# Kernel tuning notes

Hardware: AMD Instinct MI355X
Metric: run time of the kernel (lower is better)

The kernel has to match this reference:

```python
import jax, jax.numpy as jnp
import numpy as np

B, DIM, IN_DIM, H, W = 4, 512, 256, 64, 64
DOWN = IN_DIM // 2          # 128
QK = DOWN // 8              # 16
EPS = 1e-5


def conv2d(x, w, b, pad=0, dil=1):
    y = jax.lax.conv_general_dilated(
        x, w, window_strides=(1, 1),
        padding=[(pad, pad), (pad, pad)],
        rhs_dilation=(dil, dil),
        dimension_numbers=('NCHW', 'OIHW', 'NCHW'))
    return y + b[None, :, None, None]


def bn(x, g, bt, m, v):
    # inference-mode BatchNorm2d with running stats
    scale = (g * jax.lax.rsqrt(v + EPS))[None, :, None, None]
    return (x - m[None, :, None, None]) * scale + bt[None, :, None, None]


def prelu(x, a):
    return jnp.where(x >= 0, x, a * x)


def setup_inputs() -> dict:
    key = jax.random.key(0)
    ks = iter(jax.random.split(key, 64))
    d = {}
    d['x'] = jax.random.normal(next(ks), (B, DIM, H, W), dtype=jnp.float32)

    def conv_params(name, cout, cin, k):
        d[name + '_w'] = jax.random.normal(next(ks), (cout, cin, k, k), jnp.float32) * 0.05
        d[name + '_b'] = jax.random.normal(next(ks), (cout,), jnp.float32) * 0.05

    def bn_params(name, c):
        d[name + '_g'] = 1.0 + 0.1 * jax.random.normal(next(ks), (c,), jnp.float32)
        d[name + '_bt'] = 0.1 * jax.random.normal(next(ks), (c,), jnp.float32)
        d[name + '_m'] = 0.1 * jax.random.normal(next(ks), (c,), jnp.float32)
        d[name + '_v'] = 0.5 + jax.random.uniform(next(ks), (c,), jnp.float32)

    def prelu_param(name):
        d[name] = jnp.full((1,), 0.25, jnp.float32)

    conv_params('dc', IN_DIM, DIM, 3);  bn_params('dc_bn', IN_DIM); prelu_param('dc_a')
    conv_params('c1', DOWN, IN_DIM, 1); bn_params('c1_bn', DOWN);   prelu_param('c1_a')
    conv_params('c2', DOWN, IN_DIM, 3); bn_params('c2_bn', DOWN);   prelu_param('c2_a')
    conv_params('q', QK, DOWN, 1)
    conv_params('k', QK, DOWN, 1)
    conv_params('v', DOWN, DOWN, 1)
    d['gamma2'] = jnp.full((1,), 0.1, jnp.float32)  # torch init is 0; nonzero to exercise the path
    conv_params('c3', DOWN, IN_DIM, 1); bn_params('c3_bn', DOWN);   prelu_param('c3_a')
    conv_params('f', IN_DIM, 3 * DOWN, 1); bn_params('f_bn', IN_DIM); prelu_param('f_a')
    return d


def reference(x,
              dc_w, dc_b, dc_bn_g, dc_bn_bt, dc_bn_m, dc_bn_v, dc_a,
              c1_w, c1_b, c1_bn_g, c1_bn_bt, c1_bn_m, c1_bn_v, c1_a,
              c2_w, c2_b, c2_bn_g, c2_bn_bt, c2_bn_m, c2_bn_v, c2_a,
              q_w, q_b, k_w, k_b, v_w, v_b, gamma2,
              c3_w, c3_b, c3_bn_g, c3_bn_bt, c3_bn_m, c3_bn_v, c3_a,
              f_w, f_b, f_bn_g, f_bn_bt, f_bn_m, f_bn_v, f_a):
    # down_conv: 3x3 conv + BN + PReLU
    x = prelu(bn(conv2d(x, dc_w, dc_b, pad=1), dc_bn_g, dc_bn_bt, dc_bn_m, dc_bn_v), dc_a)
    # branch 1: 1x1 conv
    c1 = prelu(bn(conv2d(x, c1_w, c1_b), c1_bn_g, c1_bn_bt, c1_bn_m, c1_bn_v), c1_a)
    # branch 2: dilated 3x3 conv + non-local self-attention
    c2 = prelu(bn(conv2d(x, c2_w, c2_b, pad=2, dil=2), c2_bn_g, c2_bn_bt, c2_bn_m, c2_bn_v), c2_a)
    b, c, h, w = c2.shape
    hw = h * w
    q = conv2d(c2, q_w, q_b).reshape(b, QK, hw)   # [B, C/8, HW]
    k = conv2d(c2, k_w, k_b).reshape(b, QK, hw)
    v = conv2d(c2, v_w, v_b).reshape(b, c, hw)
    energy = jnp.einsum('bcn,bcm->bnm', q, k)     # [B, HW, HW]
    attn = jax.nn.softmax(energy, axis=-1)
    out2 = jnp.einsum('bcm,bnm->bcn', v, attn).reshape(b, c, h, w)
    out2 = gamma2 * out2 + c2
    # branch 3: global avg pool -> 1x1 conv -> broadcast (bilinear upsample of 1x1 is constant)
    pooled = jnp.mean(x, axis=(2, 3), keepdims=True)  # [B, IN_DIM, 1, 1]
    c3 = prelu(bn(conv2d(pooled, c3_w, c3_b), c3_bn_g, c3_bn_bt, c3_bn_m, c3_bn_v), c3_a)
    c3 = jnp.broadcast_to(c3, (b, DOWN, h, w))
    # fuse
    cat = jnp.concatenate([c1, out2, c3], axis=1)
    return prelu(bn(conv2d(cat, f_w, f_b), f_bn_g, f_bn_bt, f_bn_m, f_bn_v), f_a)
```

## Files before the change

### kernel.cpp

```cpp
#include <hip/hip_runtime.h>
#include <hip/hip_bf16.h>
#include <math.h>

#define HW 4096
#define EPSV 1e-5f

typedef unsigned short ushort;
typedef __attribute__((ext_vector_type(8))) short bf16x8;
typedef __attribute__((ext_vector_type(4))) float f32x4;

__device__ inline ushort f2bf(float f) {
    __hip_bfloat16 h = __float2bfloat16(f);
    return *reinterpret_cast<ushort*>(&h);
}
__device__ inline float bf2f(ushort u) {
    unsigned int v = ((unsigned int)u) << 16;
    return __uint_as_float(v);
}

template<int C>
__global__ __launch_bounds__(256) void to_chlast_bf16(
    const float* __restrict__ src, ushort* __restrict__ dst)
{
    const int b = blockIdx.z, c0 = blockIdx.y * 64, p0 = blockIdx.x * 64;
    const int tid = threadIdx.x;
    __shared__ float sT[64][65];
    for (int i = tid; i < 4096; i += 256) {
        const int ch = i >> 6, px = i & 63;
        sT[ch][px] = src[(size_t)(b * C + c0 + ch) * HW + p0 + px];
    }
    __syncthreads();
    const int px = tid >> 2, seg = tid & 3;
    ushort tmp[16];
    #pragma unroll
    for (int j = 0; j < 16; ++j) tmp[j] = f2bf(sT[seg * 16 + j][px]);
    ushort* d = dst + (size_t)(b * HW + p0 + px) * C + c0 + seg * 16;
    *(uint4*)d = *(uint4*)&tmp[0];
    *(uint4*)(d + 8) = *(uint4*)&tmp[8];
}

__global__ __launch_bounds__(256) void pack_all(
    const float* __restrict__ dc_w, ushort* __restrict__ wdcp,
    const float* __restrict__ c2_w, ushort* __restrict__ wc2p,
    const float* __restrict__ c1_w, ushort* __restrict__ wc1b,
    const float* __restrict__ f_w,  ushort* __restrict__ wfb,
    float* __restrict__ pool)
{
    constexpr int T_DC = 9 * 16 * 256 * 32;
    constexpr int T_C2 = 9 * 8 * 128 * 32;
    constexpr int T_C1 = 32768;
    constexpr int T_F  = 65536;
    int idx = blockIdx.x * 256 + threadIdx.x;
    if (idx < T_DC) {
        const int ci_in = idx & 31;
        int rest = idx >> 5;
        const int co = rest % 256; rest /= 256;
        const int cc = rest % 16;
        const int tap = rest / 16;
        wdcp[idx] = f2bf(dc_w[((size_t)co * 512 + cc * 32 + ci_in) * 9 + tap]);
        return;
    }
    idx -= T_DC;
    if (idx < T_C2) {
        const int ci_in = idx & 31;
        int rest = idx >> 5;
        const int co = rest % 128; rest /= 128;
        const int cc = rest % 8;
        const int tap = rest / 8;
        wc2p[idx] = f2bf(c2_w[((size_t)co * 256 + cc * 32 + ci_in) * 9 + tap]);
        return;
    }
    idx -= T_C2;
    if (idx < T_C1) {
        wc1b[idx] = f2bf(c1_w[idx]);
        return;
    }
    idx -= T_C1;
    if (idx < T_F) {
        const int co = idx >> 8, k = idx & 255;
        wfb[idx] = f2bf(f_w[co * 384 + k]);
        return;
    }
    idx -= T_F;
    if (idx < 1024) pool[idx] = 0.f;
}

template<int CIN, int COUT, int COTILE, int DIL, int ROWS, int OMODE>
__global__ __launch_bounds__(256, OMODE == 0 ? 4 : 2) void conv3x3_fused(
    const ushort* __restrict__ xin,
    const ushort* __restrict__ wpk,
    const float* __restrict__ bias, const float* __restrict__ bng,
    const float* __restrict__ bnb, const float* __restrict__ bnm,
    const float* __restrict__ bnv, const float* __restrict__ al,
    void* __restrict__ outv,
    float* __restrict__ pool)
{
    constexpr int HR = ROWS + 2 * DIL;
    constexpr int NC = 64 + 2 * DIL;
    constexpr int MT = COTILE / 16;
    constexpr int WPR = 4 / ROWS;
    constexpr int NT = ROWS;
    constexpr int SAS = 40;
    constexpr int CH = CIN / 32;
    constexpr int NA = HR * NC * 4;
    constexpr int NREG = (NA + 255) / 256;
    constexpr int WCH = 9 * MT * 64;
    constexpr int WPT = (WCH + 255) / 256;

    const int tid = threadIdx.x;
    const int wave = tid >> 6, lane = tid & 63;
    const int l15 = lane & 15, quad = lane >> 4;
    const int b = blockIdx.z;
    const int cob = blockIdx.y;
    const int co0 = cob * COTILE;
    const int h0 = blockIdx.x * ROWS;
    const int row = wave / WPR;
    const int ntbase = (wave % WPR) * NT;

    __shared__ __align__(16) ushort sA[HR * NC * SAS];
    __shared__ __align__(16) ushort sW[WCH * 8];

    f32x4 acc[MT][NT];
    #pragma unroll
    for (int mt = 0; mt < MT; ++mt)
        #pragma unroll
        for (int nt = 0; nt < NT; ++nt) acc[mt][nt] = (f32x4){0.f, 0.f, 0.f, 0.f};

    #pragma unroll 1
    for (int cc = 0; cc < CH; ++cc) {
        if (cc != 0) __syncthreads();
        #pragma unroll
        for (int k = 0; k < NREG; ++k) {
            const int i = tid + k * 256;
            if (i < NA) {
                const int p = i >> 2, seg = i & 3;
                const int r = p / NC, c = p - r * NC;
                const int grow = h0 - DIL + r, gcol = c - DIL;
                uint4 val = {0u, 0u, 0u, 0u};
                if (grow >= 0 && grow < 64 && gcol >= 0 && gcol < 64)
                    val = *(const uint4*)&xin[((size_t)(b * 64 + grow) * 64 + gcol) * CIN
                                              + cc * 32 + seg * 8];
                *(uint4*)&sA[p * SAS + seg * 8] = val;
            }
        }
        #pragma unroll
        for (int k = 0; k < WPT; ++k) {
            const int i = tid + k * 256;
            if (i < WCH) {
                const int tap = i / (MT * 64);
                const int r = i - tap * (MT * 64);
                const int mt = r >> 6, n = r & 63;
                const uint4 wv = *(const uint4*)&wpk[
                    ((size_t)(tap * (CIN / 32) + cc) * COUT + co0 + mt * 16 + (n & 15)) * 32
                    + (n >> 4) * 8];
                *(uint4*)&sW[i * 8] = wv;
            }
        }
        __syncthreads();

        #pragma unroll
        for (int tap = 0; tap < 9; ++tap) {
            const int ty = tap / 3, tx = tap - ty * 3;
            const int rl = row + ty * DIL;
            bf16x8 wf[MT];
            #pragma unroll
            for (int mt = 0; mt < MT; ++mt)
                wf[mt] = *(const bf16x8*)&sW[((tap * MT + mt) * 64 + lane) * 8];
            #pragma unroll
            for (int nt = 0; nt < NT; ++nt) {
                const int cl = (ntbase + nt) * 16 + l15 + tx * DIL;
                const bf16x8 bp = *(const bf16x8*)&sA[(rl * NC + cl) * SAS + quad * 8];
                #pragma unroll
                for (int mt = 0; mt < MT; ++mt)
                    acc[mt][nt] = __builtin_amdgcn_mfma_f32_16x16x32_bf16(
                        wf[mt], bp, acc[mt][nt], 0, 0, 0);
            }
        }
    }

    const float a = al[0];

    if constexpr (OMODE == 0) {
        __syncthreads();
        ushort* sT = sA;
        #pragma unroll
        for (int mt = 0; mt < MT; ++mt) {
            float sc[4], sh[4], psum[4];
            #pragma unroll
            for (int rr = 0; rr < 4; ++rr) {
                const int co = co0 + mt * 16 + quad * 4 + rr;
                sc[rr] = bng[co] * rsqrtf(bnv[co] + EPSV);
                sh[rr] = (bias[co] - bnm[co]) * sc[rr] + bnb[co];
                psum[rr] = 0.f;
            }
            #pragma unroll
            for (int nt = 0; nt < NT; ++nt) {
                float tv[4];
                #pragma unroll
                for (int rr = 0; rr < 4; ++rr) {
                    float t = acc[mt][nt][rr] * sc[rr] + sh[rr];
                    t = t >= 0.f ? t : a * t;
                    tv[rr] = t;
                    psum[rr] += t;
                }
                ushort4 u;
                u.x = f2bf(tv[0]); u.y = f2bf(tv[1]);
                u.z = f2bf(tv[2]); u.w = f2bf(tv[3]);
                const int px = (ntbase + nt) * 16 + l15;
                *(ushort4*)&sT[(row * 64 + px) * 40 + mt * 16 + quad * 4] = u;
            }
            #pragma unroll
            for (int rr = 0; rr < 4; ++rr) {
                float v = psum[rr];
                v += __shfl_xor(v, 1);
                v += __shfl_xor(v, 2);
                v += __shfl_xor(v, 4);
                v += __shfl_xor(v, 8);
                if (l15 == 0)
                    atomicAdd(&pool[b * 256 + co0 + mt * 16 + quad * 4 + rr], v);
            }
        }
        __syncthreads();
        ushort* dst = (ushort*)outv;
        const int p = tid >> 1, half = tid & 1;
        const uint4 v0 = *(const uint4*)&sT[p * 40 + half * 16];
        const uint4 v1 = *(const uint4*)&sT[p * 40 + half * 16 + 8];
        const size_t off = ((size_t)(b * 4096 + (h0 + (p >> 6)) * 64 + (p & 63))) * 256
                           + co0 + half * 16;
        *(uint4*)&dst[off] = v0;
        *(uint4*)&dst[off + 8] = v1;
    } else {
        float* out = (float*)outv;
        #pragma unroll
        for (int mt = 0; mt < MT; ++mt)
            #pragma unroll
            for (int rr = 0; rr < 4; ++rr) {
                const int co = co0 + mt * 16 + quad * 4 + rr;
                const float sc = bng[co] * rsqrtf(bnv[co] + EPSV);
                const float sh = (bias[co] - bnm[co]) * sc + bnb[co];
                #pragma unroll
                for (int nt = 0; nt < NT; ++nt) {
                    float t = acc[mt][nt][rr] * sc + sh;
                    t = t >= 0.f ? t : a * t;
                    out[((size_t)(b * COUT + co) * 64 + h0 + row) * 64
                        + (ntbase + nt) * 16 + l15] = t;
                }
            }
    }
}

template<int CIN, int COUT, bool BNACT, int OMODE>
__global__ __launch_bounds__(256) void gemm1x1_cl(
    const ushort* __restrict__ xin,
    const ushort* __restrict__ wbf,
    const float* __restrict__ bias, const float* __restrict__ bng,
    const float* __restrict__ bnb, const float* __restrict__ bnm,
    const float* __restrict__ bnv, const float* __restrict__ al,
    const float* __restrict__ ebias, void* __restrict__ outv,
    int ostride, int ocol)
{
    const int tid = threadIdx.x;
    const int wave = tid >> 6, lane = tid & 63;
    const int l15 = lane & 15, quad = lane >> 4;
    const int pix0 = blockIdx.x * 128 + wave * 32;
    const int co0 = blockIdx.y * 64;

    f32x4 acc[4][2];
    #pragma unroll
    for (int mt = 0; mt < 4; ++mt)
        #pragma unroll
        for (int nt = 0; nt < 2; ++nt) acc[mt][nt] = (f32x4){0.f, 0.f, 0.f, 0.f};

    #pragma unroll 2
    for (int cc = 0; cc < CIN / 32; ++cc) {
        bf16x8 aw[4], bp[2];
        #pragma unroll
        for (int mt = 0; mt < 4; ++mt)
            aw[mt] = *(const bf16x8*)&wbf[(size_t)(co0 + mt * 16 + l15) * CIN + cc * 32 + quad * 8];
        #pragma unroll
        for (int nt = 0; nt < 2; ++nt)
            bp[nt] = *(const bf16x8*)&xin[(size_t)(pix0 + nt * 16 + l15) * CIN + cc * 32 + quad * 8];
        #pragma unroll
        for (int mt = 0; mt < 4; ++mt)
            #pragma unroll
            for (int nt = 0; nt < 2; ++nt)
                acc[mt][nt] = __builtin_amdgcn_mfma_f32_16x16x32_bf16(
                    aw[mt], bp[nt], acc[mt][nt], 0, 0, 0);
    }

    const int bI = pix0 >> 12;
    const float a = BNACT ? al[0] : 0.f;

    if (OMODE == 0) {
        float* out = (float*)outv;
        #pragma unroll
        for (int mt = 0; mt < 4; ++mt)
            #pragma unroll
            for (int r = 0; r < 4; ++r) {
                const int co = co0 + mt * 16 + quad * 4 + r;
                float bb = bias[co];
                if (ebias) bb += ebias[bI * COUT + co];
                float scale = 1.f, shift = bb;
                if (BNACT) {
                    scale = bng[co] * rsqrtf(bnv[co] + EPSV);
                    shift = bb * scale + (bnb[co] - bnm[co] * scale);
                }
                #pragma unroll
                for (int nt = 0; nt < 2; ++nt) {
                    float t = acc[mt][nt][r] * scale + shift;
                    if (BNACT) t = t >= 0.f ? t : a * t;
                    out[((size_t)(bI * COUT + co)) * HW + (pix0 & 4095) + nt * 16 + l15] = t;
                }
            }
    } else {
        __shared__ ushort sT[4][32][68];
        #pragma unroll
        for (int mt = 0; mt < 4; ++mt)
            #pragma unroll
            for (int r = 0; r < 4; ++r) {
                const int co = co0 + mt * 16 + quad * 4 + r;
                float bb = bias[co];
                float scale = 1.f, shift = bb;
                if (BNACT) {
                    scale = bng[co] * rsqrtf(bnv[co] + EPSV);
                    shift = bb * scale + (bnb[co] - bnm[co] * scale);
                }
                #pragma unroll
                for (int nt = 0; nt < 2; ++nt) {
                    float t = acc[mt][nt][r] * scale + shift;
                    if (BNACT) t = t >= 0.f ? t : a * t;
                    sT[wave][nt * 16 + l15][mt * 16 + quad * 4 + r] = f2bf(t);
                }
            }
        __syncthreads();
        const int p = lane >> 1, half = lane & 1;
        ushort* out = (ushort*)outv;
        #pragma unroll
        for (int seg = 0; seg < 4; ++seg) {
            uint2 a0 = *(uint2*)&sT[wave][p][half * 32 + seg * 8];
            uint2 a1 = *(uint2*)&sT[wave][p][half * 32 + seg * 8 + 4];
            uint4 vv = {a0.x, a0.y, a1.x, a1.y};
            *(uint4*)&out[(size_t)(pix0 + p) * ostride + ocol + co0 + half * 32 + seg * 8] = vv;
        }
    }
}

__global__ __launch_bounds__(256) void c1_and_c3(
    const ushort* __restrict__ xin, const ushort* __restrict__ wbf,
    const float* __restrict__ bias, const float* __restrict__ bng,
    const float* __restrict__ bnb, const float* __restrict__ bnm,
    const float* __restrict__ bnv, const float* __restrict__ al,
    ushort* __restrict__ catb,
    const float* __restrict__ pool, const float* __restrict__ c3w,
    const float* __restrict__ c3b, const float* __restrict__ c3g,
    const float* __restrict__ c3bt, const float* __restrict__ c3m,
    const float* __restrict__ c3v, const float* __restrict__ c3a,
    const float* __restrict__ fw, float* __restrict__ fbias)
{
    const int tid = threadIdx.x;
    if (blockIdx.x >= 128) {
        const int b = (blockIdx.x - 128) * 2 + blockIdx.y;
        __shared__ float sp[256];
        __shared__ float sc3[128];
        sp[tid] = pool[b * 256 + tid] * (1.0f / 4096.0f);
        __syncthreads();
        if (tid < 128) {
            float acc2 = c3b[tid];
            for (int ci = 0; ci < 256; ++ci) acc2 = fmaf(c3w[tid * 256 + ci], sp[ci], acc2);
            const float scale = c3g[tid] * rsqrtf(c3v[tid] + EPSV);
            float t = (acc2 - c3m[tid]) * scale + c3bt[tid];
            const float a2 = c3a[0];
            sc3[tid] = t >= 0.f ? t : a2 * t;
        }
        __syncthreads();
        float f = 0.f;
        for (int j2 = 0; j2 < 128; ++j2) f = fmaf(fw[tid * 384 + 256 + j2], sc3[j2], f);
        fbias[b * 256 + tid] = f;
        return;
    }
    constexpr int CIN = 256;
    const int wave = tid >> 6, lane = tid & 63;
    const int l15 = lane & 15, quad = lane >> 4;
    const int pix0 = blockIdx.x * 128 + wave * 32;
    const int co0 = blockIdx.y * 64;

    f32x4 acc[4][2];
    #pragma unroll
    for (int mt = 0; mt < 4; ++mt)
        #pragma unroll
        for (int nt = 0; nt < 2; ++nt) acc[mt][nt] = (f32x4){0.f, 0.f, 0.f, 0.f};

    #pragma unroll 2
    for (int cc = 0; cc < CIN / 32; ++cc) {
        bf16x8 aw[4], bp[2];
        #pragma unroll
        for (int mt = 0; mt < 4; ++mt)
            aw[mt] = *(const bf16x8*)&wbf[(size_t)(co0 + mt * 16 + l15) * CIN + cc * 32 + quad * 8];
        #pragma unroll
        for (int nt = 0; nt < 2; ++nt)
            bp[nt] = *(const bf16x8*)&xin[(size_t)(pix0 + nt * 16 + l15) * CIN + cc * 32 + quad * 8];
        #pragma unroll
        for (int mt = 0; mt < 4; ++mt)
            #pragma unroll
            for (int nt = 0; nt < 2; ++nt)
                acc[mt][nt] = __builtin_amdgcn_mfma_f32_16x16x32_bf16(
                    aw[mt], bp[nt], acc[mt][nt], 0, 0, 0);
    }

    const float a = al[0];
    __shared__ ushort sT[4][32][68];
    #pragma unroll
    for (int mt = 0; mt < 4; ++mt)
        #pragma unroll
        for (int r = 0; r < 4; ++r) {
            const int co = co0 + mt * 16 + quad * 4 + r;
            const float scale = bng[co] * rsqrtf(bnv[co] + EPSV);
            const float shift = bias[co] * scale + (bnb[co] - bnm[co] * scale);
            #pragma unroll
            for (int nt = 0; nt < 2; ++nt) {
                float t = acc[mt][nt][r] * scale + shift;
                t = t >= 0.f ? t : a * t;
                sT[wave][nt * 16 + l15][mt * 16 + quad * 4 + r] = f2bf(t);
            }
        }
    __syncthreads();
    const int p = lane >> 1, half = lane & 1;
    #pragma unroll
    for (int seg = 0; seg < 4; ++seg) {
        uint2 a0 = *(uint2*)&sT[wave][p][half * 32 + seg * 8];
        uint2 a1 = *(uint2*)&sT[wave][p][half * 32 + seg * 8 + 4];
        uint4 vv = {a0.x, a0.y, a1.x, a1.y};
        *(uint4*)&catb[(size_t)(pix0 + p) * 256 + co0 + half * 32 + seg * 8] = vv;
    }
}

__global__ __launch_bounds__(256) void qkv_kernel(
    const float* __restrict__ c2g, const float* __restrict__ qw,
    const float* __restrict__ qb2, const float* __restrict__ kw,
    const float* __restrict__ kb2, ushort* __restrict__ qpack,
    ushort* __restrict__ kpack,
    const float* __restrict__ vw, const float* __restrict__ vb,
    ushort* __restrict__ vbh)
{
    const int tid = threadIdx.x;
    const int b = blockIdx.z, p0 = blockIdx.x * 64;
    __shared__ __align__(16) char smem[49152];

    if (blockIdx.y == 0) {
        float (*sC)[64]   = (float(*)[64])smem;
        float (*sWq)[128] = (float(*)[128])(smem + 32768);
        float (*sWk)[128] = (float(*)[128])(smem + 40960);
        for (int i = tid; i < 8192; i += 256) {
            const int px = i & 63, ci = i >> 6;
            sC[ci][px] = c2g[(size_t)(b * 128 + ci) * HW + p0 + px];
        }
        for (int i = tid; i < 2048; i += 256) {
            const int ci = i & 127, co = i >> 7;
            sWq[co][ci] = qw[co * 128 + ci];
            sWk[co][ci] = kw[co * 128 + ci];
        }
        __syncthreads();
        const int px = tid & 63, grp = tid >> 6;
        const int co0 = (grp & 1) * 8;
        const bool isK = grp >= 2;
        const float* sWp = isK ? &sWk[0][0] : &sWq[0][0];
        float acc[8] = {};
        for (int ci = 0; ci < 128; ++ci) {
            const float xv = sC[ci][px];
            #pragma unroll
            for (int j = 0; j < 8; ++j)
                acc[j] = fmaf(sWp[(co0 + j) * 128 + ci], xv, acc[j]);
        }
        const float* bsrc = isK ? kb2 : qb2;
        ushort* osrc = isK ? kpack : qpack;
        const size_t base = (size_t)(b * 4096 + p0 + px) * 32;
        #pragma unroll
        for (int j = 0; j < 8; ++j) {
            osrc[base + co0 + j] = f2bf(acc[j] + bsrc[co0 + j]);
            osrc[base + 16 + co0 + j] = 0;
        }
    } else {
        const int co0 = (blockIdx.y - 1) * 64;
        float* sIn = (float*)smem;
        float* sW  = (float*)(smem + 16384);
        const int cg = tid >> 4, pg = tid & 15;
        const int c0l = cg * 4, w0 = pg * 4;
        float acc[4][4] = {};
        for (int cc = 0; cc < 128; cc += 16) {
            {
                int i = tid;
                #pragma unroll
                for (int it = 0; it < 4; ++it, i += 256) {
                    const int px = i & 63, ci = i >> 6;
                    sIn[ci * 64 + px] = c2g[(size_t)(b * 128 + cc + ci) * HW + p0 + px];
                }
                i = tid;
                #pragma unroll
                for (int it = 0; it < 4; ++it, i += 256) {
                    const int ci = i & 15, co = i >> 4;
                    sW[ci * 68 + co] = vw[(co0 + co) * 128 + cc + ci];
                }
            }
            __syncthreads();
            #pragma unroll
            for (int ci = 0; ci < 16; ++ci) {
                const float4 iv = *(const float4*)&sIn[ci * 64 + w0];
                const float4 wv = *(const float4*)&sW[ci * 68 + c0l];
                const float ia[4] = {iv.x, iv.y, iv.z, iv.w};
                const float wa[4] = {wv.x, wv.y, wv.z, wv.w};
                #pragma unroll
                for (int i2 = 0; i2 < 4; ++i2)
                    #pragma unroll
                    for (int j = 0; j < 4; ++j)
                        acc[i2][j] = fmaf(wa[i2], ia[j], acc[i2][j]);
            }
            __syncthreads();
        }
        #pragma unroll
        for (int i2 = 0; i2 < 4; ++i2) {
            const int co = co0 + c0l + i2;
            const float shift = vb[co];
            const size_t base = (size_t)(b * 128 + co) * HW + p0 + w0;
            #pragma unroll
            for (int j = 0; j < 4; ++j)
                vbh[base + j] = f2bf(acc[i2][j] + shift);
        }
    }
}

__global__ __launch_bounds__(256) void attn_flash(
    const ushort* __restrict__ qpack,
    const ushort* __restrict__ kpack,
    const ushort* __restrict__ vpackT,
    ushort* __restrict__ opart,
    float* __restrict__ Mpart,
    float* __restrict__ Spart)
{
    const int tid = threadIdx.x;
    const int wave = tid >> 6, lane = tid & 63;
    const int l15 = lane & 15, quad = lane >> 4;
    const int b = blockIdx.z, j = blockIdx.y;
    const int n0w = blockIdx.x * 128 + wave * 32;
    const int m_begin = j * 512;

    __shared__ __align__(16) ushort sV[2][128][40];
    __shared__ __align__(16) ushort sP[4][2][16][40];

    const bf16x8 bq0 = *(const bf16x8*)(qpack + ((size_t)(b * 4096 + n0w + l15) * 32 + quad * 8));
    const bf16x8 bq1 = *(const bf16x8*)(qpack + ((size_t)(b * 4096 + n0w + 16 + l15) * 32 + quad * 8));
    const f32x4 z = {0.f, 0.f, 0.f, 0.f};

    float runM0 = -3e30f, runM1 = -3e30f;
    float runS0 = 0.f, runS1 = 0.f;
    f32x4 oacc0[8], oacc1[8];
    #pragma unroll
    for (int cs = 0; cs < 8; ++cs) {
        oacc0[cs] = (f32x4){0.f, 0.f, 0.f, 0.f};
        oacc1[cs] = (f32x4){0.f, 0.f, 0.f, 0.f};
    }

    const int stc = tid >> 1, stseg = tid & 1;

    {
        uint4 v0 = *(const uint4*)&vpackT[(size_t)(b * 128 + stc) * HW + m_begin + stseg * 16];
        uint4 v1 = *(const uint4*)&vpackT[(size_t)(b * 128 + stc) * HW + m_begin + stseg * 16 + 8];
        *(uint4*)&sV[0][stc][stseg * 16] = v0;
        *(uint4*)&sV[0][stc][stseg * 16 + 8] = v1;
    }
    __syncthreads();

    #pragma unroll 1
    for (int t = 0; t < 16; ++t) {
        const int m0 = m_begin + t * 32;
        const int buf = t & 1;
        uint4 nv0, nv1;
        const bool more = (t + 1 < 16);
        if (more) {
            const size_t nb = (size_t)(b * 128 + stc) * HW + m0 + 32 + stseg * 16;
            nv0 = *(const uint4*)&vpackT[nb];
            nv1 = *(const uint4*)&vpackT[nb + 8];
        }
        f32x4 s0[2], s1[2];
        #pragma unroll
        for (int ms = 0; ms < 2; ++ms) {
            const bf16x8 ak = *(const bf16x8*)(
                kpack + ((size_t)(b * 4096 + m0 + ms * 16 + l15) * 32 + quad * 8));
            s0[ms] = __builtin_amdgcn_mfma_f32_16x16x32_bf16(ak, bq0, z, 0, 0, 0);
            s1[ms] = __builtin_amdgcn_mfma_f32_16x16x32_bf16(ak, bq1, z, 0, 0, 0);
        }

        float tM0 = fmaxf(fmaxf(fmaxf(s0[0][0], s0[0][1]), fmaxf(s0[0][2], s0[0][3])),
                          fmaxf(fmaxf(s0[1][0], s0[1][1]), fmaxf(s0[1][2], s0[1][3])));
        float tM1 = fmaxf(fmaxf(fmaxf(s1[0][0], s1[0][1]), fmaxf(s1[0][2], s1[0][3])),
                          fmaxf(fmaxf(s1[1][0], s1[1][1]), fmaxf(s1[1][2], s1[1][3])));
        tM0 = fmaxf(tM0, __shfl_xor(tM0, 16));
        tM0 = fmaxf(tM0, __shfl_xor(tM0, 32));
        tM1 = fmaxf(tM1, __shfl_xor(tM1, 16));
        tM1 = fmaxf(tM1, __shfl_xor(tM1, 32));
        if (__any(tM0 > runM0 + 8.f)) {
            const float nM = fmaxf(runM0, tM0);
            const float sc = __builtin_amdgcn_exp2f((runM0 - nM) * 1.44269504f);
            runS0 *= sc;
            float scr[4];
            #pragma unroll
            for (int r = 0; r < 4; ++r) scr[r] = __shfl(sc, quad * 4 + r);
            #pragma unroll
            for (int cs = 0; cs < 8; ++cs) {
                oacc0[cs][0] *= scr[0]; oacc0[cs][1] *= scr[1];
                oacc0[cs][2] *= scr[2]; oacc0[cs][3] *= scr[3];
            }
            runM0 = nM;
        }
        if (__any(tM1 > runM1 + 8.f)) {
            const float nM = fmaxf(runM1, tM1);
            const float sc = __builtin_amdgcn_exp2f((runM1 - nM) * 1.44269504f);
            runS1 *= sc;
            float scr[4];
            #pragma unroll
            for (int r = 0; r < 4; ++r) scr[r] = __shfl(sc, quad * 4 + r);
            #pragma unroll
            for (int cs = 0; cs < 8; ++cs) {
                oacc1[cs][0] *= scr[0]; oacc1[cs][1] *= scr[1];
                oacc1[cs][2] *= scr[2]; oacc1[cs][3] *= scr[3];
            }
            runM1 = nM;
        }
        const float Ms0 = runM0 * 1.44269504f;
        const float Ms1 = runM1 * 1.44269504f;

        #pragma unroll
        for (int ms = 0; ms < 2; ++ms) {
            float p0[4], p1[4];
            #pragma unroll
            for (int r = 0; r < 4; ++r) {
                p0[r] = __builtin_amdgcn_exp2f(fmaf(s0[ms][r], 1.44269504f, -Ms0));
                p1[r] = __builtin_amdgcn_exp2f(fmaf(s1[ms][r], 1.44269504f, -Ms1));
                runS0 += p0[r];
                runS1 += p1[r];
            }
            ushort4 u0, u1;
            u0.x = f2bf(p0[0]); u0.y = f2bf(p0[1]); u0.z = f2bf(p0[2]); u0.w = f2bf(p0[3]);
            u1.x = f2bf(p1[0]); u1.y = f2bf(p1[1]); u1.z = f2bf(p1[2]); u1.w = f2bf(p1[3]);
            *(uint2*)&sP[wave][0][l15][ms * 16 + quad * 4] = *(uint2*)&u0;
            *(uint2*)&sP[wave][1][l15][ms * 16 + quad * 4] = *(uint2*)&u1;
        }
        asm volatile("s_waitcnt lgkmcnt(0)" ::: "memory");
        const bf16x8 ap0 = *(const bf16x8*)&sP[wave][0][l15][quad * 8];
        const bf16x8 ap1 = *(const bf16x8*)&sP[wave][1][l15][quad * 8];
        #pragma unroll
        for (int cs = 0; cs < 8; ++cs) {
            const bf16x8 bv = *(const bf16x8*)&sV[buf][cs * 16 + l15][quad * 8];
            oacc0[cs] = __builtin_amdgcn_mfma_f32_16x16x32_bf16(ap0, bv, oacc0[cs], 0, 0, 0);
            oacc1[cs] = __builtin_amdgcn_mfma_f32_16x16x32_bf16(ap1, bv, oacc1[cs], 0, 0, 0);
        }
        if (more) {
            *(uint4*)&sV[buf ^ 1][stc][stseg * 16] = nv0;
            *(uint4*)&sV[buf ^ 1][stc][stseg * 16 + 8] = nv1;
            __syncthreads();
        }
    }

    runS0 += __shfl_xor(runS0, 16);
    runS0 += __shfl_xor(runS0, 32);
    runS1 += __shfl_xor(runS1, 16);
    runS1 += __shfl_xor(runS1, 32);
    if (lane < 32) {
        const float Mv = (lane < 16) ? runM0 : runM1;
        const float Sv = (lane < 16) ? runS0 : runS1;
        const int n = n0w + ((lane < 16) ? 0 : 16) + l15;
        Mpart[((size_t)b * 8 + j) * 4096 + n] = Mv;
        Spart[((size_t)b * 8 + j) * 4096 + n] = Sv;
    }
    #pragma unroll
    for (int cs = 0; cs < 8; ++cs)
        #pragma unroll
        for (int r = 0; r < 4; ++r) {
            const int n = n0w + quad * 4 + r;
            opart[(((size_t)b * 8 + j) * 4096 + n) * 128 + cs * 16 + l15] = f2bf(oacc0[cs][r]);
            opart[(((size_t)b * 8 + j) * 4096 + n + 16) * 128 + cs * 16 + l15] = f2bf(oacc1[cs][r]);
        }
}

__global__ __launch_bounds__(256) void attn_combine(
    const ushort* __restrict__ opart, const float* __restrict__ Mpart,
    const float* __restrict__ Spart, const float* __restrict__ c2g,
    const float* __restrict__ gamma2, ushort* __restrict__ catb)
{
    const int b = blockIdx.y, n0 = blockIdx.x * 32, tid = threadIdx.x;
    __shared__ float sC2[128][33];
    __shared__ float sWj[8][32];
    if (tid < 32) {
        const int n = n0 + tid;
        float Mj[8], Sj[8];
        #pragma unroll
        for (int j = 0; j < 8; ++j) {
            Mj[j] = Mpart[((size_t)b * 8 + j) * 4096 + n];
            Sj[j] = Spart[((size_t)b * 8 + j) * 4096 + n];
        }
        float M = -3e30f;
        #pragma unroll
        for (int j = 0; j < 8; ++j) M = fmaxf(M, Mj[j]);
        float St = 0.f, e[8];
        #pragma unroll
        for (int j = 0; j < 8; ++j) { e[j] = __expf(Mj[j] - M); St += Sj[j] * e[j]; }
        const float inv = 1.0f / St;
        #pragma unroll
        for (int j = 0; j < 8; ++j) sWj[j][tid] = e[j] * inv;
    }
    #pragma unroll
    for (int e = 0; e < 16; ++e) {
        const int idx = tid + e * 256;
        const int c = idx >> 5, n = idx & 31;
        sC2[c][n] = c2g[(size_t)(b * 128 + c) * HW + n0 + n];
    }
    __syncthreads();
    const float g2 = gamma2[0];
    #pragma unroll
    for (int e = 0; e < 16; ++e) {
        const int idx = tid + e * 256;
        const int n = idx >> 7, c = idx & 127;
        float s = 0.f;
        #pragma unroll
        for (int j = 0; j < 8; ++j)
            s += bf2f(opart[(((size_t)b * 8 + j) * 4096 + n0 + n) * 128 + c]) * sWj[j][n];
        catb[(size_t)(b * 4096 + n0 + n) * 256 + 128 + c] = f2bf(fmaf(g2, s, sC2[c][n]));
    }
}

extern "C" void kernel_launch(void* const* d_in, const int* in_sizes, int n_in,
                              void* d_out, int out_size, void* d_ws, size_t ws_size,
                              hipStream_t stream)
{
    const float* x     = (const float*)d_in[0];
    const float* dc_w  = (const float*)d_in[1];
    const float* dc_b  = (const float*)d_in[2];
    const float* dc_g  = (const float*)d_in[3];
    const float* dc_bt = (const float*)d_in[4];
    const float* dc_m  = (const float*)d_in[5];
    const float* dc_v  = (const float*)d_in[6];
    const float* dc_a  = (const float*)d_in[7];
    const float* c1_w  = (const float*)d_in[8];
    const float* c1_b  = (const float*)d_in[9];
    const float* c1_g  = (const float*)d_in[10];
    const float* c1_bt = (const float*)d_in[11];
    const float* c1_m  = (const float*)d_in[12];
    const float* c1_v  = (const float*)d_in[13];
    const float* c1_a  = (const float*)d_in[14];
    const float* c2_w  = (const float*)d_in[15];
    const float* c2_b  = (const float*)d_in[16];
    const float* c2_g  = (const float*)d_in[17];
    const float* c2_bt = (const float*)d_in[18];
    const float* c2_m  = (const float*)d_in[19];
    const float* c2_v  = (const float*)d_in[20];
    const float* c2_a  = (const float*)d_in[21];
    const float* q_w   = (const float*)d_in[22];
    const float* q_b   = (const float*)d_in[23];
    const float* k_w   = (const float*)d_in[24];
    const float* k_b   = (const float*)d_in[25];
    const float* v_w   = (const float*)d_in[26];
    const float* v_b   = (const float*)d_in[27];
    const float* gamma2= (const float*)d_in[28];
    const float* c3_w  = (const float*)d_in[29];
    const float* c3_b  = (const float*)d_in[30];
    const float* c3_g  = (const float*)d_in[31];
    const float* c3_bt = (const float*)d_in[32];
    const float* c3_m  = (const float*)d_in[33];
    const float* c3_v  = (const float*)d_in[34];
    const float* c3_a  = (const float*)d_in[35];
    const float* f_w   = (const float*)d_in[36];
    const float* f_b   = (const float*)d_in[37];
    const float* f_g   = (const float*)d_in[38];
    const float* f_bt  = (const float*)d_in[39];
    const float* f_m   = (const float*)d_in[40];
    const float* f_v   = (const float*)d_in[41];
    const float* f_a   = (const float*)d_in[42];

    char* base = (char*)d_ws;
    ushort* xbf   = (ushort*)base;
    ushort* opart = (ushort*)base;
    ushort* qpk   = (ushort*)(base + 33554432);
    ushort* kpk   = (ushort*)(base + 34603008);
    ushort* vbh   = (ushort*)(base + 35651584);
    float*  c2b   = (float*)(base + 39845888);
    ushort* xpbf  = (ushort*)(base + 50331648);
    ushort* catb  = (ushort*)(base + 58720256);
    ushort* wdcp  = (ushort*)(base + 75497472);
    ushort* wc2p  = (ushort*)(base + 77856768);
    ushort* wc1b  = (ushort*)(base + 78446592);
    ushort* wfb   = (ushort*)(base + 78512128);
    float*  poolb = (float*)(base + 78643200);
    float*  fbb   = (float*)(base + 78647296);
    float*  Mpart = (float*)(base + 78651392);
    float*  Spart = (float*)(base + 79175680);

    pack_all<<<dim3(6148), 256, 0, stream>>>(
        dc_w, wdcp, c2_w, wc2p, c1_w, wc1b, f_w, wfb, poolb);
    to_chlast_bf16<512><<<dim3(64, 8, 4), 256, 0, stream>>>(x, xbf);
    conv3x3_fused<512, 256, 32, 1, 2, 0><<<dim3(32, 8, 4), 256, 0, stream>>>(
        xbf, wdcp, dc_b, dc_g, dc_bt, dc_m, dc_v, dc_a, xpbf, poolb);
    c1_and_c3<<<dim3(130, 2), 256, 0, stream>>>(
        xpbf, wc1b, c1_b, c1_g, c1_bt, c1_m, c1_v, c1_a, catb,
        poolb, c3_w, c3_b, c3_g, c3_bt, c3_m, c3_v, c3_a, f_w, fbb);
    conv3x3_fused<256, 128, 32, 2, 2, 1><<<dim3(32, 4, 4), 256, 0, stream>>>(
        xpbf, wc2p, c2_b, c2_g, c2_bt, c2_m, c2_v, c2_a, c2b, nullptr);
    qkv_kernel<<<dim3(64, 3, 4), 256, 0, stream>>>(
        c2b, q_w, q_b, k_w, k_b, qpk, kpk, v_w, v_b, vbh);
    attn_flash<<<dim3(32, 8, 4), 256, 0, stream>>>(qpk, kpk, vbh, opart, Mpart, Spart);
    attn_combine<<<dim3(128, 4), 256, 0, stream>>>(opart, Mpart, Spart, c2b, gamma2, catb);
    gemm1x1_cl<256, 256, true, 0><<<dim3(128, 4), 256, 0, stream>>>(
        catb, wfb, f_b, f_g, f_bt, f_m, f_v, f_a, fbb, (float*)d_out, 0, 0);
}
```

Baseline: 387.9 us.

## Merge weight packing with layout transpose, and c2 conv with c1/c3 branches

Folds the weight packing and the channel-last bf16 conversion of x into one launch. It also merges the dilated 3x3 c2 convolution with the c1 1x1 GEMM and the c3 pooled-branch kernel into a single launch, routing by block index. The aim is to remove two kernel launches and let the independent branches run concurrently on the device instead of one after another. The cost is a larger shared-memory footprint and register pressure applied to every block, and some idle blocks in the merged grid.

```diff
diff --git a/kernel.cpp b/kernel.cpp
--- a/kernel.cpp
+++ b/kernel.cpp
@@ -18,71 +18,72 @@
     return __uint_as_float(v);
 }
 
-template<int C>
-__global__ __launch_bounds__(256) void to_chlast_bf16(
-    const float* __restrict__ src, ushort* __restrict__ dst)
+__global__ __launch_bounds__(256) void pack_and_chlast(
+    const float* __restrict__ dc_w, ushort* __restrict__ wdcp,
+    const float* __restrict__ c2_w, ushort* __restrict__ wc2p,
+    const float* __restrict__ c1_w, ushort* __restrict__ wc1b,
+    const float* __restrict__ f_w,  ushort* __restrict__ wfb,
+    float* __restrict__ pool,
+    const float* __restrict__ x, ushort* __restrict__ xbf)
 {
-    const int b = blockIdx.z, c0 = blockIdx.y * 64, p0 = blockIdx.x * 64;
+    constexpr int PACK_BLKS = 6148;
+    constexpr int T_DC = 9 * 16 * 256 * 32;
+    constexpr int T_C2 = 9 * 8 * 128 * 32;
+    constexpr int T_C1 = 32768;
+    constexpr int T_F  = 65536;
     const int tid = threadIdx.x;
     __shared__ float sT[64][65];
+
+    if (blockIdx.x < PACK_BLKS) {
+        int idx = blockIdx.x * 256 + tid;
+        if (idx < T_DC) {
+            const int ci_in = idx & 31;
+            int rest = idx >> 5;
+            const int co = rest % 256; rest /= 256;
+            const int cc = rest % 16;
+            const int tap = rest / 16;
+            wdcp[idx] = f2bf(dc_w[((size_t)co * 512 + cc * 32 + ci_in) * 9 + tap]);
+            return;
+        }
+        idx -= T_DC;
+        if (idx < T_C2) {
+            const int ci_in = idx & 31;
+            int rest = idx >> 5;
+            const int co = rest % 128; rest /= 128;
+            const int cc = rest % 8;
+            const int tap = rest / 8;
+            wc2p[idx] = f2bf(c2_w[((size_t)co * 256 + cc * 32 + ci_in) * 9 + tap]);
+            return;
+        }
+        idx -= T_C2;
+        if (idx < T_C1) { wc1b[idx] = f2bf(c1_w[idx]); return; }
+        idx -= T_C1;
+        if (idx < T_F) {
+            const int co = idx >> 8, k = idx & 255;
+            wfb[idx] = f2bf(f_w[co * 384 + k]);
+            return;
+        }
+        idx -= T_F;
+        if (idx < 1024) pool[idx] = 0.f;
+        return;
+    }
+
+    const int f = blockIdx.x - PACK_BLKS;
+    const int p0 = (f & 63) * 64;
+    const int c0 = ((f >> 6) & 7) * 64;
+    const int b  = f >> 9;
     for (int i = tid; i < 4096; i += 256) {
         const int ch = i >> 6, px = i & 63;
-        sT[ch][px] = src[(size_t)(b * C + c0 + ch) * HW + p0 + px];
+        sT[ch][px] = x[(size_t)(b * 512 + c0 + ch) * HW + p0 + px];
     }
     __syncthreads();
     const int px = tid >> 2, seg = tid & 3;
     ushort tmp[16];
     #pragma unroll
     for (int j = 0; j < 16; ++j) tmp[j] = f2bf(sT[seg * 16 + j][px]);
-    ushort* d = dst + (size_t)(b * HW + p0 + px) * C + c0 + seg * 16;
+    ushort* d = xbf + (size_t)(b * HW + p0 + px) * 512 + c0 + seg * 16;
     *(uint4*)d = *(uint4*)&tmp[0];
     *(uint4*)(d + 8) = *(uint4*)&tmp[8];
-}
-
-__global__ __launch_bounds__(256) void pack_all(
-    const float* __restrict__ dc_w, ushort* __restrict__ wdcp,
-    const float* __restrict__ c2_w, ushort* __restrict__ wc2p,
-    const float* __restrict__ c1_w, ushort* __restrict__ wc1b,
-    const float* __restrict__ f_w,  ushort* __restrict__ wfb,
-    float* __restrict__ pool)
-{
-    constexpr int T_DC = 9 * 16 * 256 * 32;
-    constexpr int T_C2 = 9 * 8 * 128 * 32;
-    constexpr int T_C1 = 32768;
-    constexpr int T_F  = 65536;
-    int idx = blockIdx.x * 256 + threadIdx.x;
-    if (idx < T_DC) {
-        const int ci_in = idx & 31;
-        int rest = idx >> 5;
-        const int co = rest % 256; rest /= 256;
-        const int cc = rest % 16;
-        const int tap = rest / 16;
-        wdcp[idx] = f2bf(dc_w[((size_t)co * 512 + cc * 32 + ci_in) * 9 + tap]);
-        return;
-    }
-    idx -= T_DC;
-    if (idx < T_C2) {
-        const int ci_in = idx & 31;
-        int rest = idx >> 5;
-        const int co = rest % 128; rest /= 128;
-        const int cc = rest % 8;
-        const int tap = rest / 8;
-        wc2p[idx] = f2bf(c2_w[((size_t)co * 256 + cc * 32 + ci_in) * 9 + tap]);
-        return;
-    }
-    idx -= T_C2;
-    if (idx < T_C1) {
-        wc1b[idx] = f2bf(c1_w[idx]);
-        return;
-    }
-    idx -= T_C1;
-    if (idx < T_F) {
-        const int co = idx >> 8, k = idx & 255;
-        wfb[idx] = f2bf(f_w[co * 384 + k]);
-        return;
-    }
-    idx -= T_F;
-    if (idx < 1024) pool[idx] = 0.f;
 }
 
 template<int CIN, int COUT, int COTILE, int DIL, int ROWS, int OMODE>
@@ -249,6 +250,210 @@
     }
 }
 
+__global__ __launch_bounds__(256, 2) void c2_c1_c3(
+    const ushort* __restrict__ xin,
+    const ushort* __restrict__ wpk,
+    const float* __restrict__ c2bias, const float* __restrict__ c2gn,
+    const float* __restrict__ c2bt, const float* __restrict__ c2mn,
+    const float* __restrict__ c2vr, const float* __restrict__ c2al,
+    float* __restrict__ c2out,
+    const ushort* __restrict__ wbf,
+    const float* __restrict__ bias, const float* __restrict__ bng,
+    const float* __restrict__ bnb, const float* __restrict__ bnm,
+    const float* __restrict__ bnv, const float* __restrict__ al,
+    ushort* __restrict__ catb,
+    const float* __restrict__ pool, const float* __restrict__ c3w,
+    const float* __restrict__ c3b, const float* __restrict__ c3g,
+    const float* __restrict__ c3bt, const float* __restrict__ c3m,
+    const float* __restrict__ c3v, const float* __restrict__ c3a,
+    const float* __restrict__ fw, float* __restrict__ fbias)
+{
+    const int tid = threadIdx.x;
+    const int wave = tid >> 6, lane = tid & 63;
+    const int l15 = lane & 15, quad = lane >> 4;
+    __shared__ __align__(16) char smem[51072];
+
+    if (blockIdx.x < 32) {
+        constexpr int CIN = 256, COUT = 128, COTILE = 32, DIL = 2, ROWS = 2;
+        constexpr int HR = ROWS + 2 * DIL;
+        constexpr int NC = 64 + 2 * DIL;
+        constexpr int MT = COTILE / 16;
+        constexpr int WPR = 4 / ROWS;
+        constexpr int NT = ROWS;
+        constexpr int SAS = 40;
+        constexpr int CH = CIN / 32;
+        constexpr int NA = HR * NC * 4;
+        constexpr int NREG = (NA + 255) / 256;
+        constexpr int WCH = 9 * MT * 64;
+        constexpr int WPT = (WCH + 255) / 256;
+
+        ushort* sA = (ushort*)smem;
+        ushort* sW = (ushort*)(smem + 32640);
+
+        const int b = blockIdx.z;
+        const int co0 = blockIdx.y * COTILE;
+        const int h0 = blockIdx.x * ROWS;
+        const int row = wave / WPR;
+        const int ntbase = (wave % WPR) * NT;
+
+        f32x4 acc[MT][NT];
+        #pragma unroll
+        for (int mt = 0; mt < MT; ++mt)
+            #pragma unroll
+            for (int nt = 0; nt < NT; ++nt) acc[mt][nt] = (f32x4){0.f, 0.f, 0.f, 0.f};
+
+        #pragma unroll 1
+        for (int cc = 0; cc < CH; ++cc) {
+            if (cc != 0) __syncthreads();
+            #pragma unroll
+            for (int k = 0; k < NREG; ++k) {
+                const int i = tid + k * 256;
+                if (i < NA) {
+                    const int p = i >> 2, seg = i & 3;
+                    const int r = p / NC, c = p - r * NC;
+                    const int grow = h0 - DIL + r, gcol = c - DIL;
+                    uint4 val = {0u, 0u, 0u, 0u};
+                    if (grow >= 0 && grow < 64 && gcol >= 0 && gcol < 64)
+                        val = *(const uint4*)&xin[((size_t)(b * 64 + grow) * 64 + gcol) * CIN
+                                                  + cc * 32 + seg * 8];
+                    *(uint4*)&sA[p * SAS + seg * 8] = val;
+                }
+            }
+            #pragma unroll
+            for (int k = 0; k < WPT; ++k) {
+                const int i = tid + k * 256;
+                if (i < WCH) {
+                    const int tap = i / (MT * 64);
+                    const int r = i - tap * (MT * 64);
+                    const int mt = r >> 6, n = r & 63;
+                    const uint4 wv = *(const uint4*)&wpk[
+                        ((size_t)(tap * (CIN / 32) + cc) * COUT + co0 + mt * 16 + (n & 15)) * 32
+                        + (n >> 4) * 8];
+                    *(uint4*)&sW[i * 8] = wv;
+                }
+            }
+            __syncthreads();
+
+            #pragma unroll
+            for (int tap = 0; tap < 9; ++tap) {
+                const int ty = tap / 3, tx = tap - ty * 3;
+                const int rl = row + ty * DIL;
+                bf16x8 wf[MT];
+                #pragma unroll
+                for (int mt = 0; mt < MT; ++mt)
+                    wf[mt] = *(const bf16x8*)&sW[((tap * MT + mt) * 64 + lane) * 8];
+                #pragma unroll
+                for (int nt = 0; nt < NT; ++nt) {
+                    const int cl = (ntbase + nt) * 16 + l15 + tx * DIL;
+                    const bf16x8 bp = *(const bf16x8*)&sA[(rl * NC + cl) * SAS + quad * 8];
+                    #pragma unroll
+                    for (int mt = 0; mt < MT; ++mt)
+                        acc[mt][nt] = __builtin_amdgcn_mfma_f32_16x16x32_bf16(
+                            wf[mt], bp, acc[mt][nt], 0, 0, 0);
+                }
+            }
+        }
+
+        const float a = c2al[0];
+        #pragma unroll
+        for (int mt = 0; mt < MT; ++mt)
+            #pragma unroll
+            for (int rr = 0; rr < 4; ++rr) {
+                const int co = co0 + mt * 16 + quad * 4 + rr;
+                const float sc = c2gn[co] * rsqrtf(c2vr[co] + EPSV);
+                const float sh = (c2bias[co] - c2mn[co]) * sc + c2bt[co];
+                #pragma unroll
+                for (int nt = 0; nt < NT; ++nt) {
+                    float t = acc[mt][nt][rr] * sc + sh;
+                    t = t >= 0.f ? t : a * t;
+                    c2out[((size_t)(b * COUT + co) * 64 + h0 + row) * 64
+                          + (ntbase + nt) * 16 + l15] = t;
+                }
+            }
+        return;
+    }
+
+    const int flat = (blockIdx.z * 4 + blockIdx.y) * 17 + (blockIdx.x - 32);
+    if (flat >= 260) return;
+    const int bx = flat % 130, by = flat / 130;
+
+    if (bx >= 128) {
+        const int b = (bx - 128) * 2 + by;
+        float* sp  = (float*)smem;
+        float* sc3 = (float*)(smem + 2048);
+        sp[tid] = pool[b * 256 + tid] * (1.0f / 4096.0f);
+        __syncthreads();
+        if (tid < 128) {
+            float acc2 = c3b[tid];
+            for (int ci = 0; ci < 256; ++ci) acc2 = fmaf(c3w[tid * 256 + ci], sp[ci], acc2);
+            const float scale = c3g[tid] * rsqrtf(c3v[tid] + EPSV);
+            float t = (acc2 - c3m[tid]) * scale + c3bt[tid];
+            const float a2 = c3a[0];
+            sc3[tid] = t >= 0.f ? t : a2 * t;
+        }
+        __syncthreads();
+        float f = 0.f;
+        for (int j2 = 0; j2 < 128; ++j2) f = fmaf(fw[tid * 384 + 256 + j2], sc3[j2], f);
+        fbias[b * 256 + tid] = f;
+        return;
+    }
+
+    {
+        constexpr int CIN = 256;
+        const int pix0 = bx * 128 + wave * 32;
+        const int co0 = by * 64;
+
+        f32x4 acc[4][2];
+        #pragma unroll
+        for (int mt = 0; mt < 4; ++mt)
+            #pragma unroll
+            for (int nt = 0; nt < 2; ++nt) acc[mt][nt] = (f32x4){0.f, 0.f, 0.f, 0.f};
+
+        #pragma unroll 2
+        for (int cc = 0; cc < CIN / 32; ++cc) {
+            bf16x8 aw[4], bp[2];
+            #pragma unroll
+            for (int mt = 0; mt < 4; ++mt)
+                aw[mt] = *(const bf16x8*)&wbf[(size_t)(co0 + mt * 16 + l15) * CIN + cc * 32 + quad * 8];
+            #pragma unroll
+            for (int nt = 0; nt < 2; ++nt)
+                bp[nt] = *(const bf16x8*)&xin[(size_t)(pix0 + nt * 16 + l15) * CIN + cc * 32 + quad * 8];
+            #pragma unroll
+            for (int mt = 0; mt < 4; ++mt)
+                #pragma unroll
+                for (int nt = 0; nt < 2; ++nt)
+                    acc[mt][nt] = __builtin_amdgcn_mfma_f32_16x16x32_bf16(
+                        aw[mt], bp[nt], acc[mt][nt], 0, 0, 0);
+        }
+
+        const float a = al[0];
+        ushort* sT = (ushort*)smem;
+        #pragma unroll
+        for (int mt = 0; mt < 4; ++mt)
+            #pragma unroll
+            for (int r = 0; r < 4; ++r) {
+                const int co = co0 + mt * 16 + quad * 4 + r;
+                const float scale = bng[co] * rsqrtf(bnv[co] + EPSV);
+                const float shift = bias[co] * scale + (bnb[co] - bnm[co] * scale);
+                #pragma unroll
+                for (int nt = 0; nt < 2; ++nt) {
+                    float t = acc[mt][nt][r] * scale + shift;
+                    t = t >= 0.f ? t : a * t;
+                    sT[((wave * 32 + nt * 16 + l15) * 68) + mt * 16 + quad * 4 + r] = f2bf(t);
+                }
+            }
+        __syncthreads();
+        const int p = lane >> 1, half = lane & 1;
+        #pragma unroll
+        for (int seg = 0; seg < 4; ++seg) {
+            uint2 a0 = *(uint2*)&sT[((wave * 32 + p) * 68) + half * 32 + seg * 8];
+            uint2 a1 = *(uint2*)&sT[((wave * 32 + p) * 68) + half * 32 + seg * 8 + 4];
+            uint4 vv = {a0.x, a0.y, a1.x, a1.y};
+            *(uint4*)&catb[(size_t)(pix0 + p) * 256 + co0 + half * 32 + seg * 8] = vv;
+        }
+    }
+}
+
 template<int CIN, int COUT, bool BNACT, int OMODE>
 __global__ __launch_bounds__(256) void gemm1x1_cl(
     const ushort* __restrict__ xin,
@@ -342,95 +547,6 @@
             uint4 vv = {a0.x, a0.y, a1.x, a1.y};
             *(uint4*)&out[(size_t)(pix0 + p) * ostride + ocol + co0 + half * 32 + seg * 8] = vv;
         }
-    }
-}
-
-__global__ __launch_bounds__(256) void c1_and_c3(
-    const ushort* __restrict__ xin, const ushort* __restrict__ wbf,
-    const float* __restrict__ bias, const float* __restrict__ bng,
-    const float* __restrict__ bnb, const float* __restrict__ bnm,
-    const float* __restrict__ bnv, const float* __restrict__ al,
-    ushort* __restrict__ catb,
-    const float* __restrict__ pool, const float* __restrict__ c3w,
-    const float* __restrict__ c3b, const float* __restrict__ c3g,
-    const float* __restrict__ c3bt, const float* __restrict__ c3m,
-    const float* __restrict__ c3v, const float* __restrict__ c3a,
-    const float* __restrict__ fw, float* __restrict__ fbias)
-{
-    const int tid = threadIdx.x;
-    if (blockIdx.x >= 128) {
-        const int b = (blockIdx.x - 128) * 2 + blockIdx.y;
-        __shared__ float sp[256];
-        __shared__ float sc3[128];
-        sp[tid] = pool[b * 256 + tid] * (1.0f / 4096.0f);
-        __syncthreads();
-        if (tid < 128) {
-            float acc2 = c3b[tid];
-            for (int ci = 0; ci < 256; ++ci) acc2 = fmaf(c3w[tid * 256 + ci], sp[ci], acc2);
-            const float scale = c3g[tid] * rsqrtf(c3v[tid] + EPSV);
-            float t = (acc2 - c3m[tid]) * scale + c3bt[tid];
-            const float a2 = c3a[0];
-            sc3[tid] = t >= 0.f ? t : a2 * t;
-        }
-        __syncthreads();
-        float f = 0.f;
-        for (int j2 = 0; j2 < 128; ++j2) f = fmaf(fw[tid * 384 + 256 + j2], sc3[j2], f);
-        fbias[b * 256 + tid] = f;
-        return;
-    }
-    constexpr int CIN = 256;
-    const int wave = tid >> 6, lane = tid & 63;
-    const int l15 = lane & 15, quad = lane >> 4;
-    const int pix0 = blockIdx.x * 128 + wave * 32;
-    const int co0 = blockIdx.y * 64;
-
-    f32x4 acc[4][2];
-    #pragma unroll
-    for (int mt = 0; mt < 4; ++mt)
-        #pragma unroll
-        for (int nt = 0; nt < 2; ++nt) acc[mt][nt] = (f32x4){0.f, 0.f, 0.f, 0.f};
-
-    #pragma unroll 2
-    for (int cc = 0; cc < CIN / 32; ++cc) {
-        bf16x8 aw[4], bp[2];
-        #pragma unroll
-        for (int mt = 0; mt < 4; ++mt)
-            aw[mt] = *(const bf16x8*)&wbf[(size_t)(co0 + mt * 16 + l15) * CIN + cc * 32 + quad * 8];
-        #pragma unroll
-        for (int nt = 0; nt < 2; ++nt)
-            bp[nt] = *(const bf16x8*)&xin[(size_t)(pix0 + nt * 16 + l15) * CIN + cc * 32 + quad * 8];
-        #pragma unroll
-        for (int mt = 0; mt < 4; ++mt)
-            #pragma unroll
-            for (int nt = 0; nt < 2; ++nt)
-                acc[mt][nt] = __builtin_amdgcn_mfma_f32_16x16x32_bf16(
-                    aw[mt], bp[nt], acc[mt][nt], 0, 0, 0);
-    }
-
-    const float a = al[0];
-    __shared__ ushort sT[4][32][68];
-    #pragma unroll
-    for (int mt = 0; mt < 4; ++mt)
-        #pragma unroll
-        for (int r = 0; r < 4; ++r) {
-            const int co = co0 + mt * 16 + quad * 4 + r;
-            const float scale = bng[co] * rsqrtf(bnv[co] + EPSV);
-            const float shift = bias[co] * scale + (bnb[co] - bnm[co] * scale);
-            #pragma unroll
-            for (int nt = 0; nt < 2; ++nt) {
-                float t = acc[mt][nt][r] * scale + shift;
-                t = t >= 0.f ? t : a * t;
-                sT[wave][nt * 16 + l15][mt * 16 + quad * 4 + r] = f2bf(t);
-            }
-        }
-    __syncthreads();
-    const int p = lane >> 1, half = lane & 1;
-    #pragma unroll
-    for (int seg = 0; seg < 4; ++seg) {
-        uint2 a0 = *(uint2*)&sT[wave][p][half * 32 + seg * 8];
-        uint2 a1 = *(uint2*)&sT[wave][p][half * 32 + seg * 8 + 4];
-        uint4 vv = {a0.x, a0.y, a1.x, a1.y};
-        *(uint4*)&catb[(size_t)(pix0 + p) * 256 + co0 + half * 32 + seg * 8] = vv;
     }
 }
 
@@ -793,16 +909,14 @@
     float*  Mpart = (float*)(base + 78651392);
     float*  Spart = (float*)(base + 79175680);
 
-    pack_all<<<dim3(6148), 256, 0, stream>>>(
-        dc_w, wdcp, c2_w, wc2p, c1_w, wc1b, f_w, wfb, poolb);
-    to_chlast_bf16<512><<<dim3(64, 8, 4), 256, 0, stream>>>(x, xbf);
+    pack_and_chlast<<<dim3(6148 + 2048), 256, 0, stream>>>(
+        dc_w, wdcp, c2_w, wc2p, c1_w, wc1b, f_w, wfb, poolb, x, xbf);
     conv3x3_fused<512, 256, 32, 1, 2, 0><<<dim3(32, 8, 4), 256, 0, stream>>>(
         xbf, wdcp, dc_b, dc_g, dc_bt, dc_m, dc_v, dc_a, xpbf, poolb);
-    c1_and_c3<<<dim3(130, 2), 256, 0, stream>>>(
-        xpbf, wc1b, c1_b, c1_g, c1_bt, c1_m, c1_v, c1_a, catb,
+    c2_c1_c3<<<dim3(49, 4, 4), 256, 0, stream>>>(
+        xpbf, wc2p, c2_b, c2_g, c2_bt, c2_m, c2_v, c2_a, c2b,
+        wc1b, c1_b, c1_g, c1_bt, c1_m, c1_v, c1_a, catb,
         poolb, c3_w, c3_b, c3_g, c3_bt, c3_m, c3_v, c3_a, f_w, fbb);
-    conv3x3_fused<256, 128, 32, 2, 2, 1><<<dim3(32, 4, 4), 256, 0, stream>>>(
-        xpbf, wc2p, c2_b, c2_g, c2_bt, c2_m, c2_v, c2_a, c2b, nullptr);
     qkv_kernel<<<dim3(64, 3, 4), 256, 0, stream>>>(
         c2b, q_w, q_b, k_w, k_b, qpk, kpk, v_w, v_b, vbh);
     attn_flash<<<dim3(32, 8, 4), 256, 0, stream>>>(qpk, kpk, vbh, opart, Mpart, Spart);
```

Result: faster. 374.4 us (-3.5%).
